# Optimization experiments

Measured on AMD Instinct MI355X. Metric: run time of the kernel, lower is better.

The kernel has to match this reference:

```python
import jax, jax.numpy as jnp
import numpy as np

B, L, D = 4, 2048, 256
DI, DS, DCONV, DTR, K = 512, 16, 4, 16, 3  # d_inner, d_state, mamba conv, dt_rank, outer conv kernel
PAD = 1 * (K - 1)  # dilation*(kernel_size-1)
ALPHA = 0.5


def setup_inputs() -> dict:
    key = jax.random.key(0)
    ks = jax.random.split(key, 14)
    s = lambda k, shape, scale: jax.random.normal(k, shape, dtype=jnp.float32) * scale
    inp = {
        "x": s(ks[0], (B, L, D), 1.0),
        "ln_w": jnp.ones((D,), jnp.float32),
        "ln_b": jnp.zeros((D,), jnp.float32),
        "conv_w": s(ks[1], (D, D, K), 0.05),          # outer Conv1d weight (out,in,k)
        "conv_b": s(ks[2], (D,), 0.02),
        "in_proj_w": s(ks[3], (2 * DI, D), 0.05),      # Mamba in_proj (no bias)
        "conv1d_w": s(ks[4], (DI, 1, DCONV), 0.3),     # depthwise causal conv
        "conv1d_b": s(ks[5], (DI,), 0.02),
        "x_proj_w": s(ks[6], (DTR + 2 * DS, DI), 0.05),
        "dt_proj_w": s(ks[7], (DI, DTR), 0.1),
        "dt_proj_b": s(ks[8], (DI,), 0.1),
        "A_log": jnp.log(jnp.broadcast_to(jnp.arange(1, DS + 1, dtype=jnp.float32), (DI, DS))),
        "D_param": jnp.ones((DI,), jnp.float32),
        "out_proj_w": s(ks[9], (D, DI), 0.05),
    }
    return inp


def _layernorm(h, w, b):
    mu = jnp.mean(h, axis=-1, keepdims=True)
    var = jnp.mean(jnp.square(h - mu), axis=-1, keepdims=True)
    return (h - mu) * jax.lax.rsqrt(var + 1e-5) * w + b


def _causal_conv(h_ncl, w, pad, groups):
    # h_ncl: (B, C, L); left-pad only -> output length L (matches pad-then-slice in torch)
    return jax.lax.conv_general_dilated(
        h_ncl, w, window_strides=(1,), padding=[(pad, 0)],
        dimension_numbers=("NCH", "OIH", "NCH"), feature_group_count=groups)


def _mamba(h, in_proj_w, conv1d_w, conv1d_b, x_proj_w, dt_proj_w, dt_proj_b, A_log, D_param, out_proj_w):
    xz = jnp.einsum("bld,ed->ble", h, in_proj_w)          # (B,L,2*DI)
    xin, z = jnp.split(xz, 2, axis=-1)
    xc = _causal_conv(xin.transpose(0, 2, 1), conv1d_w, DCONV - 1, DI)
    xc = jax.nn.silu(xc + conv1d_b[None, :, None]).transpose(0, 2, 1)   # (B,L,DI)
    x_dbl = jnp.einsum("bld,ed->ble", xc, x_proj_w)
    dt, Bm, Cm = jnp.split(x_dbl, [DTR, DTR + DS], axis=-1)
    delta = jax.nn.softplus(jnp.einsum("blr,dr->bld", dt, dt_proj_w) + dt_proj_b)  # (B,L,DI)
    A = -jnp.exp(A_log)                                     # (DI,DS)
    dA = jnp.exp(delta[..., None] * A)                      # (B,L,DI,DS)
    dBx = delta[..., None] * Bm[:, :, None, :] * xc[..., None]

    def step(hst, t):
        dA_t, dBx_t, C_t = t
        hst = dA_t * hst + dBx_t                            # (B,DI,DS)
        y = jnp.einsum("bds,bs->bd", hst, C_t)
        return hst, y

    h0 = jnp.zeros((h.shape[0], DI, DS), h.dtype)
    _, ys = jax.lax.scan(step, h0, (dA.transpose(1, 0, 2, 3), dBx.transpose(1, 0, 2, 3), Cm.transpose(1, 0, 2)))
    y = ys.transpose(1, 0, 2) + xc * D_param                # (B,L,DI)
    y = y * jax.nn.silu(z)
    return jnp.einsum("ble,de->bld", y, out_proj_w)


def reference(x, ln_w, ln_b, conv_w, conv_b, in_proj_w, conv1d_w, conv1d_b,
              x_proj_w, dt_proj_w, dt_proj_b, A_log, D_param, out_proj_w):
    h = _layernorm(x, ln_w, ln_b)
    # conv branch: pad left, conv, GELU (exact erf, as torch nn.GELU)
    hc = _causal_conv(h.transpose(0, 2, 1), conv_w, PAD, 1) + conv_b[None, :, None]
    h_conv = jax.nn.gelu(hc, approximate=False).transpose(0, 2, 1)
    h_mamba = _mamba(h, in_proj_w, conv1d_w, conv1d_b, x_proj_w, dt_proj_w,
                     dt_proj_b, A_log, D_param, out_proj_w)
    h_out = ALPHA * h_mamba + (1.0 - ALPHA) * h_conv
    return x + h_out
```

## Files before the change

kernel.cpp:

```cpp
#include <hip/hip_runtime.h>
#include <math.h>

#define BBATCH 4
#define LSEQ   2048
#define DMODEL 256
#define DINNER 512
#define DSTATE 16
#define DTRANK 16
#define MROWS  (BBATCH * LSEQ)
#define NCHUNK 64
#define LCHUNK (LSEQ / NCHUNK)

typedef unsigned short u16;
typedef __attribute__((ext_vector_type(8))) short bf16x8;
typedef __attribute__((ext_vector_type(4))) float f32x4;

#define OFF_HBF    ((size_t)0)
#define OFF_HCONV  ((size_t)1048576)
#define OFF_XIN    ((size_t)3145728)
#define OFF_XPART  ((size_t)5242880)
#define OFF_Z      ((size_t)7340032)
#define OFF_XC     ((size_t)11534336)
#define OFF_DELTA  ((size_t)15728640)
#define OFF_XDBL   ((size_t)19922944)
#define OFF_YBF    ((size_t)20316160)
#define OFF_AAGG   ((size_t)22413312)
#define OFF_BAGG   ((size_t)24510464)
#define OFF_HINIT  OFF_AAGG
#define OFF_WTINBF ((size_t)26607616)
#define OFF_WTCVBF ((size_t)26738688)
#define OFF_WTOUTBF ((size_t)26836992)
#define OFF_WTX    ((size_t)26902528)
#define OFF_WTDT   ((size_t)26927104)

__device__ __forceinline__ float silu_f(float v) {
  return v / (1.0f + __expf(-v));
}
__device__ __forceinline__ u16 f2bf(float f) {
  unsigned u = __float_as_uint(f);
  return (u16)((u + 0x7FFFu + ((u >> 16) & 1u)) >> 16);
}
__device__ __forceinline__ float bf2f(u16 v) {
  return __uint_as_float(((unsigned)v) << 16);
}

__global__ __launch_bounds__(256) void k_repack(
    const float* __restrict__ inw, const float* __restrict__ convw,
    const float* __restrict__ xw, const float* __restrict__ dtw,
    const float* __restrict__ ow, float* __restrict__ ws) {
  int idx = blockIdx.x * 256 + threadIdx.x;
  u16* win  = (u16*)(ws + OFF_WTINBF);
  u16* wcv  = (u16*)(ws + OFF_WTCVBF);
  u16* wout = (u16*)(ws + OFF_WTOUTBF);
  float* wx  = ws + OFF_WTX;
  float* wdt = ws + OFF_WTDT;
  if (idx < 262144) {
    win[idx] = f2bf(inw[idx]);
    return;
  }
  int i2 = idx - 262144;
  if (i2 < 196608) {
    int o = i2 / 768, r = i2 - o * 768;
    int kk = r >> 8, i = r & 255;
    wcv[i2] = f2bf(convw[(o * 256 + i) * 3 + kk]);
    return;
  }
  int i3 = i2 - 196608;
  if (i3 < 131072) {
    wout[i3] = f2bf(ow[i3]);
    return;
  }
  int i4 = i3 - 131072;
  if (i4 < 24576) {
    int k = i4 / 48, n = i4 - k * 48;
    wx[i4] = xw[n * 512 + k];
    return;
  }
  int i5 = i4 - 24576;
  if (i5 < 8192) {
    int r = i5 >> 9, n = i5 & 511;
    wdt[i5] = dtw[n * 16 + r];
  }
}

__global__ __launch_bounds__(256) void k_layernorm(
    const float* __restrict__ x, const float* __restrict__ w,
    const float* __restrict__ b, u16* __restrict__ hb) {
  int wave = threadIdx.x >> 6;
  int lane = threadIdx.x & 63;
  int row  = blockIdx.x * 4 + wave;
  const float4* xr = reinterpret_cast<const float4*>(x + (size_t)row * 256);
  float4 v = xr[lane];
  float s  = v.x + v.y + v.z + v.w;
  float sq = v.x*v.x + v.y*v.y + v.z*v.z + v.w*v.w;
  #pragma unroll
  for (int o = 32; o >= 1; o >>= 1) { s += __shfl_xor(s, o); sq += __shfl_xor(sq, o); }
  float mu  = s * (1.0f / 256.0f);
  float var = sq * (1.0f / 256.0f) - mu * mu;
  float rs  = rsqrtf(var + 1e-5f);
  float4 wv = reinterpret_cast<const float4*>(w)[lane];
  float4 bv = reinterpret_cast<const float4*>(b)[lane];
  ushort4 o4;
  o4.x = f2bf((v.x - mu) * rs * wv.x + bv.x);
  o4.y = f2bf((v.y - mu) * rs * wv.y + bv.y);
  o4.z = f2bf((v.z - mu) * rs * wv.z + bv.z);
  o4.w = f2bf((v.w - mu) * rs * wv.w + bv.w);
  reinterpret_cast<ushort4*>(hb + (size_t)row * 256)[lane] = o4;
}


__global__ __launch_bounds__(256) void k_bgemm_inproj(
    const u16* __restrict__ Abf, const u16* __restrict__ Bbf,
    u16* __restrict__ xin, u16* __restrict__ z) {
  __shared__ __align__(16) u16 As[64 * 72];
  __shared__ __align__(16) u16 Bs[128 * 72];
  int tid = threadIdx.x;
  int m0 = blockIdx.x * 64, n0 = blockIdx.y * 128;
  int lane = tid & 63, wid = tid >> 6;
  int wc = wid * 32;
  int l15 = lane & 15, lk = (lane >> 4) * 8;
  int r0 = tid >> 3, kc = (tid & 7) * 8;
  f32x4 acc[4][2] = {};
  for (int k0 = 0; k0 < 256; k0 += 64) {
    *(bf16x8*)&As[r0 * 72 + kc] =
        *(const bf16x8*)&Abf[(size_t)(m0 + r0) * 256 + k0 + kc];
    *(bf16x8*)&As[(r0 + 32) * 72 + kc] =
        *(const bf16x8*)&Abf[(size_t)(m0 + r0 + 32) * 256 + k0 + kc];
    #pragma unroll
    for (int rr = 0; rr < 4; ++rr)
      *(bf16x8*)&Bs[(r0 + rr * 32) * 72 + kc] =
          *(const bf16x8*)&Bbf[(size_t)(n0 + r0 + rr * 32) * 256 + k0 + kc];
    __syncthreads();
    #pragma unroll
    for (int kk = 0; kk < 64; kk += 32) {
      bf16x8 b0 = *(const bf16x8*)&Bs[(wc + l15) * 72 + kk + lk];
      bf16x8 b1 = *(const bf16x8*)&Bs[(wc + 16 + l15) * 72 + kk + lk];
      #pragma unroll
      for (int q = 0; q < 4; ++q) {
        bf16x8 a = *(const bf16x8*)&As[(q * 16 + l15) * 72 + kk + lk];
        acc[q][0] = __builtin_amdgcn_mfma_f32_16x16x32_bf16(a, b0, acc[q][0], 0, 0, 0);
        acc[q][1] = __builtin_amdgcn_mfma_f32_16x16x32_bf16(a, b1, acc[q][1], 0, 0, 0);
      }
    }
    __syncthreads();
  }
  u16* dst = (blockIdx.y < 4) ? xin : z;
  int nb = n0 & 511;
  int rsub = (lane >> 4) * 4;
  #pragma unroll
  for (int q = 0; q < 4; ++q)
    #pragma unroll
    for (int ni = 0; ni < 2; ++ni) {
      int gc = nb + wc + ni * 16 + l15;
      #pragma unroll
      for (int r = 0; r < 4; ++r)
        dst[(size_t)(m0 + q * 16 + rsub + r) * 512 + gc] = f2bf(acc[q][ni][r]);
    }
}

__global__ __launch_bounds__(256) void k_bgemm_conv(
    const u16* __restrict__ hbf, const u16* __restrict__ Bbf,
    const float* __restrict__ cb, float* __restrict__ hconv) {
  __shared__ __align__(16) u16 As[64 * 72];
  __shared__ __align__(16) u16 Bs[64 * 72];
  int tid = threadIdx.x;
  int m0 = blockIdx.x * 64, n0 = blockIdx.y * 64;
  int bidx = m0 >> 11, t0 = m0 & 2047;
  int lane = tid & 63, wid = tid >> 6;
  int wr = (wid >> 1) * 32, wc = (wid & 1) * 32;
  int l15 = lane & 15, lk = (lane >> 4) * 8;
  int r0 = tid >> 3, kc = (tid & 7) * 8;
  f32x4 acc[2][2] = {};
  for (int k0 = 0; k0 < 768; k0 += 64) {
    int kkc = k0 >> 8;
    int i0  = (k0 & 255) + kc;
    int t1  = t0 + r0 - 2 + kkc;
    bf16x8 av0 = {0, 0, 0, 0, 0, 0, 0, 0};
    if (t1 >= 0)
      av0 = *(const bf16x8*)&hbf[(size_t)((bidx << 11) + t1) * 256 + i0];
    bf16x8 av1 =
        *(const bf16x8*)&hbf[(size_t)((bidx << 11) + t1 + 32) * 256 + i0];
    *(bf16x8*)&As[r0 * 72 + kc] = av0;
    *(bf16x8*)&As[(r0 + 32) * 72 + kc] = av1;
    *(bf16x8*)&Bs[r0 * 72 + kc] =
        *(const bf16x8*)&Bbf[(size_t)(n0 + r0) * 768 + k0 + kc];
    *(bf16x8*)&Bs[(r0 + 32) * 72 + kc] =
        *(const bf16x8*)&Bbf[(size_t)(n0 + r0 + 32) * 768 + k0 + kc];
    __syncthreads();
    #pragma unroll
    for (int kk = 0; kk < 64; kk += 32) {
      bf16x8 a0 = *(const bf16x8*)&As[(wr + l15) * 72 + kk + lk];
      bf16x8 a1 = *(const bf16x8*)&As[(wr + 16 + l15) * 72 + kk + lk];
      bf16x8 b0 = *(const bf16x8*)&Bs[(wc + l15) * 72 + kk + lk];
      bf16x8 b1 = *(const bf16x8*)&Bs[(wc + 16 + l15) * 72 + kk + lk];
      acc[0][0] = __builtin_amdgcn_mfma_f32_16x16x32_bf16(a0, b0, acc[0][0], 0, 0, 0);
      acc[0][1] = __builtin_amdgcn_mfma_f32_16x16x32_bf16(a0, b1, acc[0][1], 0, 0, 0);
      acc[1][0] = __builtin_amdgcn_mfma_f32_16x16x32_bf16(a1, b0, acc[1][0], 0, 0, 0);
      acc[1][1] = __builtin_amdgcn_mfma_f32_16x16x32_bf16(a1, b1, acc[1][1], 0, 0, 0);
    }
    __syncthreads();
  }
  int rowb = m0 + wr + (lane >> 4) * 4;
  #pragma unroll
  for (int mi = 0; mi < 2; ++mi)
    #pragma unroll
    for (int ni = 0; ni < 2; ++ni) {
      int gc = n0 + wc + ni * 16 + l15;
      float bias = cb[gc];
      #pragma unroll
      for (int r = 0; r < 4; ++r) {
        float v = acc[mi][ni][r] + bias;
        float g = 0.5f * v * (1.0f + erff(v * 0.70710678118654752440f));
        hconv[(size_t)(rowb + mi * 16 + r) * 256 + gc] = g;
      }
    }
}

__global__ __launch_bounds__(256) void k_bgemm_outproj(
    const u16* __restrict__ Abf, const u16* __restrict__ Bbf,
    const float* __restrict__ x, const float* __restrict__ hconv,
    float* __restrict__ out) {
  __shared__ __align__(16) u16 As[64 * 72];
  __shared__ __align__(16) u16 Bs[64 * 72];
  int tid = threadIdx.x;
  int m0 = blockIdx.x * 64, n0 = blockIdx.y * 64;
  int lane = tid & 63, wid = tid >> 6;
  int wr = (wid >> 1) * 32, wc = (wid & 1) * 32;
  int l15 = lane & 15, lk = (lane >> 4) * 8;
  int r0 = tid >> 3, kc = (tid & 7) * 8;
  f32x4 acc[2][2] = {};
  for (int k0 = 0; k0 < 512; k0 += 64) {
    *(bf16x8*)&As[r0 * 72 + kc] =
        *(const bf16x8*)&Abf[(size_t)(m0 + r0) * 512 + k0 + kc];
    *(bf16x8*)&As[(r0 + 32) * 72 + kc] =
        *(const bf16x8*)&Abf[(size_t)(m0 + r0 + 32) * 512 + k0 + kc];
    *(bf16x8*)&Bs[r0 * 72 + kc] =
        *(const bf16x8*)&Bbf[(size_t)(n0 + r0) * 512 + k0 + kc];
    *(bf16x8*)&Bs[(r0 + 32) * 72 + kc] =
        *(const bf16x8*)&Bbf[(size_t)(n0 + r0 + 32) * 512 + k0 + kc];
    __syncthreads();
    #pragma unroll
    for (int kk = 0; kk < 64; kk += 32) {
      bf16x8 a0 = *(const bf16x8*)&As[(wr + l15) * 72 + kk + lk];
      bf16x8 a1 = *(const bf16x8*)&As[(wr + 16 + l15) * 72 + kk + lk];
      bf16x8 b0 = *(const bf16x8*)&Bs[(wc + l15) * 72 + kk + lk];
      bf16x8 b1 = *(const bf16x8*)&Bs[(wc + 16 + l15) * 72 + kk + lk];
      acc[0][0] = __builtin_amdgcn_mfma_f32_16x16x32_bf16(a0, b0, acc[0][0], 0, 0, 0);
      acc[0][1] = __builtin_amdgcn_mfma_f32_16x16x32_bf16(a0, b1, acc[0][1], 0, 0, 0);
      acc[1][0] = __builtin_amdgcn_mfma_f32_16x16x32_bf16(a1, b0, acc[1][0], 0, 0, 0);
      acc[1][1] = __builtin_amdgcn_mfma_f32_16x16x32_bf16(a1, b1, acc[1][1], 0, 0, 0);
    }
    __syncthreads();
  }
  int rowb = m0 + wr + (lane >> 4) * 4;
  #pragma unroll
  for (int mi = 0; mi < 2; ++mi)
    #pragma unroll
    for (int ni = 0; ni < 2; ++ni) {
      int gc = n0 + wc + ni * 16 + l15;
      #pragma unroll
      for (int r = 0; r < 4; ++r) {
        size_t off = (size_t)(rowb + mi * 16 + r) * 256 + gc;
        out[off] = x[off] + 0.5f * acc[mi][ni][r] + 0.5f * hconv[off];
      }
    }
}

__global__ __launch_bounds__(256) void k_xproj_part(
    const float* __restrict__ A, const float* __restrict__ Bt,
    float* __restrict__ Cpart) {
  __shared__ float As[16][68];
  __shared__ float Bs[16][68];
  int tid = threadIdx.x;
  int m0 = blockIdx.x * 64;
  int kc = blockIdx.y;
  int ar = tid >> 2, ac = (tid & 3) * 4;
  int br = tid >> 4, bc = (tid & 15) * 4;
  int tx = tid & 15, ty = tid >> 4;
  float acc[4][4] = {};
  for (int k0 = kc * 128; k0 < kc * 128 + 128; k0 += 16) {
    float4 av = *reinterpret_cast<const float4*>(A + (size_t)(m0 + ar) * 512 + k0 + ac);
    As[ac + 0][ar] = av.x; As[ac + 1][ar] = av.y;
    As[ac + 2][ar] = av.z; As[ac + 3][ar] = av.w;
    float4 bv = make_float4(0.f, 0.f, 0.f, 0.f);
    if (bc < 48)
      bv = *reinterpret_cast<const float4*>(Bt + (size_t)(k0 + br) * 48 + bc);
    *reinterpret_cast<float4*>(&Bs[br][bc]) = bv;
    __syncthreads();
    #pragma unroll
    for (int kt = 0; kt < 16; ++kt) {
      float4 a = *reinterpret_cast<const float4*>(&As[kt][ty * 4]);
      float4 b = *reinterpret_cast<const float4*>(&Bs[kt][tx * 4]);
      acc[0][0]+=a.x*b.x; acc[0][1]+=a.x*b.y; acc[0][2]+=a.x*b.z; acc[0][3]+=a.x*b.w;
      acc[1][0]+=a.y*b.x; acc[1][1]+=a.y*b.y; acc[1][2]+=a.y*b.z; acc[1][3]+=a.y*b.w;
      acc[2][0]+=a.z*b.x; acc[2][1]+=a.z*b.y; acc[2][2]+=a.z*b.z; acc[2][3]+=a.z*b.w;
      acc[3][0]+=a.w*b.x; acc[3][1]+=a.w*b.y; acc[3][2]+=a.w*b.z; acc[3][3]+=a.w*b.w;
    }
    __syncthreads();
  }
  float* C = Cpart + (size_t)kc * (MROWS * 48);
  if (tx < 12) {
    #pragma unroll
    for (int i = 0; i < 4; ++i) {
      float4 cv = make_float4(acc[i][0], acc[i][1], acc[i][2], acc[i][3]);
      *reinterpret_cast<float4*>(C + (size_t)(m0 + ty * 4 + i) * 48 + tx * 4) = cv;
    }
  }
}

__global__ __launch_bounds__(256) void k_xproj_sum(
    const float* __restrict__ Cpart, float* __restrict__ C) {
  int idx = blockIdx.x * 256 + threadIdx.x;
  const size_t S = (size_t)MROWS * 48;
  C[idx] = ((Cpart[idx] + Cpart[S + idx]) + Cpart[2 * S + idx]) + Cpart[3 * S + idx];
}

__global__ __launch_bounds__(256) void k_dtproj(
    const float* __restrict__ xdbl, const float* __restrict__ Wdt,
    const float* __restrict__ db, float* __restrict__ delta) {
  __shared__ float dts[4][17];
  int tid = threadIdx.x;
  int m0 = blockIdx.x * 4;
  if (tid < 64) {
    int rr = tid >> 4, cc = tid & 15;
    dts[rr][cc] = xdbl[(size_t)(m0 + rr) * 48 + cc];
  }
  __syncthreads();
  float wv0[16], wv1[16];
  #pragma unroll
  for (int r = 0; r < 16; ++r) {
    wv0[r] = Wdt[r * 512 + tid];
    wv1[r] = Wdt[r * 512 + tid + 256];
  }
  float b0 = db[tid], b1 = db[tid + 256];
  #pragma unroll
  for (int m = 0; m < 4; ++m) {
    float a0 = b0, a1 = b1;
    #pragma unroll
    for (int r = 0; r < 16; ++r) {
      float d = dts[m][r];
      a0 += d * wv0[r];
      a1 += d * wv1[r];
    }
    delta[(size_t)(m0 + m) * 512 + tid]       = (a0 > 20.0f) ? a0 : log1pf(__expf(a0));
    delta[(size_t)(m0 + m) * 512 + tid + 256] = (a1 > 20.0f) ? a1 : log1pf(__expf(a1));
  }
}

__global__ __launch_bounds__(256) void k_dwconv(
    const u16* __restrict__ xin, const float* __restrict__ cw,
    const float* __restrict__ cb, float* __restrict__ xc) {
  int idx = blockIdx.x * 256 + threadIdx.x;
  int di = idx & 511;
  int m  = idx >> 9;
  int t  = m & 2047;
  float w0 = cw[di * 4 + 0], w1 = cw[di * 4 + 1];
  float w2 = cw[di * 4 + 2], w3 = cw[di * 4 + 3];
  const u16* base = xin + (size_t)m * 512 + di;
  float acc = cb[di] + w3 * bf2f(base[0]);
  if (t >= 1) acc += w2 * bf2f(base[-512]);
  if (t >= 2) acc += w1 * bf2f(base[-1024]);
  if (t >= 3) acc += w0 * bf2f(base[-1536]);
  xc[(size_t)m * 512 + di] = silu_f(acc);
}

__global__ __launch_bounds__(256) void k_scan1(
    const float* __restrict__ delta, const float* __restrict__ xdbl,
    const float* __restrict__ xc, const float* __restrict__ Alog,
    float* __restrict__ Aagg, float* __restrict__ Bagg) {
  int di = ((blockIdx.x & 1) << 8) | threadIdx.x;
  int c  = (blockIdx.x >> 1) & 63;
  int b  = blockIdx.x >> 7;
  float nA[16];
  #pragma unroll
  for (int q = 0; q < 4; ++q) {
    float4 v = *reinterpret_cast<const float4*>(Alog + (size_t)di * 16 + q * 4);
    nA[q*4+0] = -__expf(v.x); nA[q*4+1] = -__expf(v.y);
    nA[q*4+2] = -__expf(v.z); nA[q*4+3] = -__expf(v.w);
  }
  float ap[16], bacc[16];
  #pragma unroll
  for (int s = 0; s < 16; ++s) { ap[s] = 1.0f; bacc[s] = 0.0f; }
  int row0 = b * 2048 + c * LCHUNK;
  const float* dp = delta + (size_t)row0 * 512 + di;
  const float* xp = xc    + (size_t)row0 * 512 + di;
  const float* Bp = xdbl  + (size_t)row0 * 48 + 16;
  #pragma unroll 2
  for (int t = 0; t < LCHUNK; ++t) {
    float dv = dp[t * 512];
    float u  = dv * xp[t * 512];
    #pragma unroll
    for (int s = 0; s < 16; ++s) {
      float e = __expf(dv * nA[s]);
      ap[s]   *= e;
      bacc[s]  = e * bacc[s] + u * Bp[t * 48 + s];
    }
  }
  size_t base = ((size_t)((b * 64 + c) * 16)) * 512 + di;
  #pragma unroll
  for (int s = 0; s < 16; ++s) {
    Aagg[base + (size_t)s * 512] = ap[s];
    Bagg[base + (size_t)s * 512] = bacc[s];
  }
}

__global__ __launch_bounds__(256) void k_scan2(
    const float* __restrict__ Aagg, const float* __restrict__ Bagg,
    float* __restrict__ Hinit) {
  int g  = blockIdx.x * 256 + threadIdx.x;
  int di = g & 511, s = (g >> 9) & 15, b = g >> 13;
  float h = 0.0f;
  for (int c = 0; c < NCHUNK; ++c) {
    size_t idx = ((size_t)((b * 64 + c) * 16 + s)) * 512 + di;
    float a = Aagg[idx], bb = Bagg[idx];
    Hinit[idx] = h;
    h = a * h + bb;
  }
}

__global__ __launch_bounds__(256) void k_scan3(
    const float* __restrict__ delta, const float* __restrict__ xdbl,
    const float* __restrict__ xc, const u16* __restrict__ z,
    const float* __restrict__ Alog, const float* __restrict__ Dp,
    const float* __restrict__ Hinit, u16* __restrict__ y) {
  int di = ((blockIdx.x & 1) << 8) | threadIdx.x;
  int c  = (blockIdx.x >> 1) & 63;
  int b  = blockIdx.x >> 7;
  float nA[16];
  #pragma unroll
  for (int q = 0; q < 4; ++q) {
    float4 v = *reinterpret_cast<const float4*>(Alog + (size_t)di * 16 + q * 4);
    nA[q*4+0] = -__expf(v.x); nA[q*4+1] = -__expf(v.y);
    nA[q*4+2] = -__expf(v.z); nA[q*4+3] = -__expf(v.w);
  }
  float h[16];
  size_t hb = ((size_t)((b * 64 + c) * 16)) * 512 + di;
  #pragma unroll
  for (int s = 0; s < 16; ++s) h[s] = Hinit[hb + (size_t)s * 512];
  float Dv = Dp[di];
  int row0 = b * 2048 + c * LCHUNK;
  const float* dp = delta + (size_t)row0 * 512 + di;
  const float* xp = xc    + (size_t)row0 * 512 + di;
  const u16*   zp = z     + (size_t)row0 * 512 + di;
  const float* Bp = xdbl  + (size_t)row0 * 48 + 16;
  const float* Cp = xdbl  + (size_t)row0 * 48 + 32;
  u16* yp         = y     + (size_t)row0 * 512 + di;
  #pragma unroll 2
  for (int t = 0; t < LCHUNK; ++t) {
    float dv  = dp[t * 512];
    float xcv = xp[t * 512];
    float u   = dv * xcv;
    float yv  = 0.0f;
    #pragma unroll
    for (int s = 0; s < 16; ++s) {
      float e = __expf(dv * nA[s]);
      h[s] = e * h[s] + u * Bp[t * 48 + s];
      yv  += h[s] * Cp[t * 48 + s];
    }
    yv += xcv * Dv;
    float zv = bf2f(zp[t * 512]);
    yp[t * 512] = f2bf(yv * silu_f(zv));
  }
}

extern "C" void kernel_launch(void* const* d_in, const int* in_sizes, int n_in,
                              void* d_out, int out_size, void* d_ws, size_t ws_size,
                              hipStream_t stream) {
  const float* x     = (const float*)d_in[0];
  const float* lnw   = (const float*)d_in[1];
  const float* lnb   = (const float*)d_in[2];
  const float* convw = (const float*)d_in[3];
  const float* convb = (const float*)d_in[4];
  const float* inw   = (const float*)d_in[5];
  const float* c1w   = (const float*)d_in[6];
  const float* c1b   = (const float*)d_in[7];
  const float* xw    = (const float*)d_in[8];
  const float* dtw   = (const float*)d_in[9];
  const float* dtb   = (const float*)d_in[10];
  const float* alog  = (const float*)d_in[11];
  const float* Dp    = (const float*)d_in[12];
  const float* ow    = (const float*)d_in[13];
  float* ws  = (float*)d_ws;
  float* out = (float*)d_out;

  u16* hbf     = (u16*)(ws + OFF_HBF);
  float* hconv = ws + OFF_HCONV;
  u16* xinbf   = (u16*)(ws + OFF_XIN);
  float* xpart = ws + OFF_XPART;
  u16* zbf     = (u16*)(ws + OFF_Z);
  float* xc    = ws + OFF_XC;
  float* delta = ws + OFF_DELTA;
  float* xdbl  = ws + OFF_XDBL;
  u16* ybf     = (u16*)(ws + OFF_YBF);
  float* Aagg  = ws + OFF_AAGG;
  float* Bagg  = ws + OFF_BAGG;
  float* Hinit = ws + OFF_HINIT;
  u16* winbf   = (u16*)(ws + OFF_WTINBF);
  u16* wcvbf   = (u16*)(ws + OFF_WTCVBF);
  u16* woutbf  = (u16*)(ws + OFF_WTOUTBF);
  float* Wtx   = ws + OFF_WTX;
  float* Wtdt  = ws + OFF_WTDT;

  k_repack<<<2432, 256, 0, stream>>>(inw, convw, xw, dtw, ow, ws);
  k_layernorm<<<2048, 256, 0, stream>>>(x, lnw, lnb, hbf);
  k_bgemm_conv<<<dim3(128, 4), 256, 0, stream>>>(hbf, wcvbf, convb, hconv);
  k_bgemm_inproj<<<dim3(128, 8), 256, 0, stream>>>(hbf, winbf, xinbf, zbf);
  k_dwconv<<<16384, 256, 0, stream>>>(xinbf, c1w, c1b, xc);
  k_xproj_part<<<dim3(128, 4), 256, 0, stream>>>(xc, Wtx, xpart);
  k_xproj_sum<<<1536, 256, 0, stream>>>(xpart, xdbl);
  k_dtproj<<<2048, 256, 0, stream>>>(xdbl, Wtdt, dtb, delta);
  k_scan1<<<512, 256, 0, stream>>>(delta, xdbl, xc, alog, Aagg, Bagg);
  k_scan2<<<128, 256, 0, stream>>>(Aagg, Bagg, Hinit);
  k_scan3<<<512, 256, 0, stream>>>(delta, xdbl, xc, zbf, alog, Dp, Hinit, ybf);
  k_bgemm_outproj<<<dim3(128, 4), 256, 0, stream>>>(ybf, woutbf, x, hconv, out);
}
```

Before: 237.9 us.

## Merge layernorm with weight repack, fuse conv/inproj GEMMs, fold xproj reduction into dtproj

Three launch-level fusions. Layernorm and weight repacking now run as one grid split by block index. The conv-branch GEMM and the in_proj GEMM run as one grid, also split by block index. The split-K partial sum for x_proj is folded into the dt_proj kernel, which also writes xdbl. This removes three kernel launches, the gaps between them, and one intermediate pass over the x_proj partials. The risk is that the merged GEMM kernel now reserves the larger shared-memory footprint for conv blocks as well, which could lower occupancy.

Result: faster. 218.9 us (-8.0%).

```diff
diff --git a/kernel.cpp b/kernel.cpp
--- a/kernel.cpp
+++ b/kernel.cpp
@@ -44,11 +44,36 @@
   return __uint_as_float(((unsigned)v) << 16);
 }
 
-__global__ __launch_bounds__(256) void k_repack(
+__global__ __launch_bounds__(256) void k_ln_repack(
+    const float* __restrict__ x, const float* __restrict__ lnw,
+    const float* __restrict__ lnb, u16* __restrict__ hb,
     const float* __restrict__ inw, const float* __restrict__ convw,
     const float* __restrict__ xw, const float* __restrict__ dtw,
     const float* __restrict__ ow, float* __restrict__ ws) {
-  int idx = blockIdx.x * 256 + threadIdx.x;
+  if (blockIdx.x < 2048) {
+    int wave = threadIdx.x >> 6;
+    int lane = threadIdx.x & 63;
+    int row  = blockIdx.x * 4 + wave;
+    const float4* xr = reinterpret_cast<const float4*>(x + (size_t)row * 256);
+    float4 v = xr[lane];
+    float s  = v.x + v.y + v.z + v.w;
+    float sq = v.x*v.x + v.y*v.y + v.z*v.z + v.w*v.w;
+    #pragma unroll
+    for (int o = 32; o >= 1; o >>= 1) { s += __shfl_xor(s, o); sq += __shfl_xor(sq, o); }
+    float mu  = s * (1.0f / 256.0f);
+    float var = sq * (1.0f / 256.0f) - mu * mu;
+    float rs  = rsqrtf(var + 1e-5f);
+    float4 wv = reinterpret_cast<const float4*>(lnw)[lane];
+    float4 bv = reinterpret_cast<const float4*>(lnb)[lane];
+    ushort4 o4;
+    o4.x = f2bf((v.x - mu) * rs * wv.x + bv.x);
+    o4.y = f2bf((v.y - mu) * rs * wv.y + bv.y);
+    o4.z = f2bf((v.z - mu) * rs * wv.z + bv.z);
+    o4.w = f2bf((v.w - mu) * rs * wv.w + bv.w);
+    reinterpret_cast<ushort4*>(hb + (size_t)row * 256)[lane] = o4;
+    return;
+  }
+  int idx = (blockIdx.x - 2048) * 256 + threadIdx.x;
   u16* win  = (u16*)(ws + OFF_WTINBF);
   u16* wcv  = (u16*)(ws + OFF_WTCVBF);
   u16* wout = (u16*)(ws + OFF_WTOUTBF);
@@ -83,53 +108,82 @@
   }
 }
 
-__global__ __launch_bounds__(256) void k_layernorm(
-    const float* __restrict__ x, const float* __restrict__ w,
-    const float* __restrict__ b, u16* __restrict__ hb) {
-  int wave = threadIdx.x >> 6;
-  int lane = threadIdx.x & 63;
-  int row  = blockIdx.x * 4 + wave;
-  const float4* xr = reinterpret_cast<const float4*>(x + (size_t)row * 256);
-  float4 v = xr[lane];
-  float s  = v.x + v.y + v.z + v.w;
-  float sq = v.x*v.x + v.y*v.y + v.z*v.z + v.w*v.w;
-  #pragma unroll
-  for (int o = 32; o >= 1; o >>= 1) { s += __shfl_xor(s, o); sq += __shfl_xor(sq, o); }
-  float mu  = s * (1.0f / 256.0f);
-  float var = sq * (1.0f / 256.0f) - mu * mu;
-  float rs  = rsqrtf(var + 1e-5f);
-  float4 wv = reinterpret_cast<const float4*>(w)[lane];
-  float4 bv = reinterpret_cast<const float4*>(b)[lane];
-  ushort4 o4;
-  o4.x = f2bf((v.x - mu) * rs * wv.x + bv.x);
-  o4.y = f2bf((v.y - mu) * rs * wv.y + bv.y);
-  o4.z = f2bf((v.z - mu) * rs * wv.z + bv.z);
-  o4.w = f2bf((v.w - mu) * rs * wv.w + bv.w);
-  reinterpret_cast<ushort4*>(hb + (size_t)row * 256)[lane] = o4;
-}
-
-
-__global__ __launch_bounds__(256) void k_bgemm_inproj(
-    const u16* __restrict__ Abf, const u16* __restrict__ Bbf,
-    u16* __restrict__ xin, u16* __restrict__ z) {
+
+__global__ __launch_bounds__(256) void k_bgemm_both(
+    const u16* __restrict__ hbf, const u16* __restrict__ Bcv,
+    const float* __restrict__ cb, float* __restrict__ hconv,
+    const u16* __restrict__ Bin, u16* __restrict__ xin, u16* __restrict__ z) {
   __shared__ __align__(16) u16 As[64 * 72];
   __shared__ __align__(16) u16 Bs[128 * 72];
+  int blk = blockIdx.x;
   int tid = threadIdx.x;
-  int m0 = blockIdx.x * 64, n0 = blockIdx.y * 128;
   int lane = tid & 63, wid = tid >> 6;
-  int wc = wid * 32;
   int l15 = lane & 15, lk = (lane >> 4) * 8;
   int r0 = tid >> 3, kc = (tid & 7) * 8;
+  if (blk < 512) {
+    int m0 = (blk & 127) * 64, n0 = (blk >> 7) * 64;
+    int bidx = m0 >> 11, t0 = m0 & 2047;
+    int wr = (wid >> 1) * 32, wc = (wid & 1) * 32;
+    f32x4 acc[2][2] = {};
+    for (int k0 = 0; k0 < 768; k0 += 64) {
+      int kkc = k0 >> 8;
+      int i0  = (k0 & 255) + kc;
+      int t1  = t0 + r0 - 2 + kkc;
+      bf16x8 av0 = {0, 0, 0, 0, 0, 0, 0, 0};
+      if (t1 >= 0)
+        av0 = *(const bf16x8*)&hbf[(size_t)((bidx << 11) + t1) * 256 + i0];
+      bf16x8 av1 =
+          *(const bf16x8*)&hbf[(size_t)((bidx << 11) + t1 + 32) * 256 + i0];
+      *(bf16x8*)&As[r0 * 72 + kc] = av0;
+      *(bf16x8*)&As[(r0 + 32) * 72 + kc] = av1;
+      *(bf16x8*)&Bs[r0 * 72 + kc] =
+          *(const bf16x8*)&Bcv[(size_t)(n0 + r0) * 768 + k0 + kc];
+      *(bf16x8*)&Bs[(r0 + 32) * 72 + kc] =
+          *(const bf16x8*)&Bcv[(size_t)(n0 + r0 + 32) * 768 + k0 + kc];
+      __syncthreads();
+      #pragma unroll
+      for (int kk = 0; kk < 64; kk += 32) {
+        bf16x8 a0 = *(const bf16x8*)&As[(wr + l15) * 72 + kk + lk];
+        bf16x8 a1 = *(const bf16x8*)&As[(wr + 16 + l15) * 72 + kk + lk];
+        bf16x8 b0 = *(const bf16x8*)&Bs[(wc + l15) * 72 + kk + lk];
+        bf16x8 b1 = *(const bf16x8*)&Bs[(wc + 16 + l15) * 72 + kk + lk];
+        acc[0][0] = __builtin_amdgcn_mfma_f32_16x16x32_bf16(a0, b0, acc[0][0], 0, 0, 0);
+        acc[0][1] = __builtin_amdgcn_mfma_f32_16x16x32_bf16(a0, b1, acc[0][1], 0, 0, 0);
+        acc[1][0] = __builtin_amdgcn_mfma_f32_16x16x32_bf16(a1, b0, acc[1][0], 0, 0, 0);
+        acc[1][1] = __builtin_amdgcn_mfma_f32_16x16x32_bf16(a1, b1, acc[1][1], 0, 0, 0);
+      }
+      __syncthreads();
+    }
+    int rowb = m0 + wr + (lane >> 4) * 4;
+    #pragma unroll
+    for (int mi = 0; mi < 2; ++mi)
+      #pragma unroll
+      for (int ni = 0; ni < 2; ++ni) {
+        int gc = n0 + wc + ni * 16 + l15;
+        float bias = cb[gc];
+        #pragma unroll
+        for (int r = 0; r < 4; ++r) {
+          float v = acc[mi][ni][r] + bias;
+          float g = 0.5f * v * (1.0f + erff(v * 0.70710678118654752440f));
+          hconv[(size_t)(rowb + mi * 16 + r) * 256 + gc] = g;
+        }
+      }
+    return;
+  }
+  int bid = blk - 512;
+  int m0 = (bid & 127) * 64, ny = bid >> 7;
+  int n0 = ny * 128;
+  int wc = wid * 32;
   f32x4 acc[4][2] = {};
   for (int k0 = 0; k0 < 256; k0 += 64) {
     *(bf16x8*)&As[r0 * 72 + kc] =
-        *(const bf16x8*)&Abf[(size_t)(m0 + r0) * 256 + k0 + kc];
+        *(const bf16x8*)&hbf[(size_t)(m0 + r0) * 256 + k0 + kc];
     *(bf16x8*)&As[(r0 + 32) * 72 + kc] =
-        *(const bf16x8*)&Abf[(size_t)(m0 + r0 + 32) * 256 + k0 + kc];
+        *(const bf16x8*)&hbf[(size_t)(m0 + r0 + 32) * 256 + k0 + kc];
     #pragma unroll
     for (int rr = 0; rr < 4; ++rr)
       *(bf16x8*)&Bs[(r0 + rr * 32) * 72 + kc] =
-          *(const bf16x8*)&Bbf[(size_t)(n0 + r0 + rr * 32) * 256 + k0 + kc];
+          *(const bf16x8*)&Bin[(size_t)(n0 + r0 + rr * 32) * 256 + k0 + kc];
     __syncthreads();
     #pragma unroll
     for (int kk = 0; kk < 64; kk += 32) {
@@ -144,7 +198,7 @@
     }
     __syncthreads();
   }
-  u16* dst = (blockIdx.y < 4) ? xin : z;
+  u16* dst = (ny < 4) ? xin : z;
   int nb = n0 & 511;
   int rsub = (lane >> 4) * 4;
   #pragma unroll
@@ -155,64 +209,6 @@
       #pragma unroll
       for (int r = 0; r < 4; ++r)
         dst[(size_t)(m0 + q * 16 + rsub + r) * 512 + gc] = f2bf(acc[q][ni][r]);
-    }
-}
-
-__global__ __launch_bounds__(256) void k_bgemm_conv(
-    const u16* __restrict__ hbf, const u16* __restrict__ Bbf,
-    const float* __restrict__ cb, float* __restrict__ hconv) {
-  __shared__ __align__(16) u16 As[64 * 72];
-  __shared__ __align__(16) u16 Bs[64 * 72];
-  int tid = threadIdx.x;
-  int m0 = blockIdx.x * 64, n0 = blockIdx.y * 64;
-  int bidx = m0 >> 11, t0 = m0 & 2047;
-  int lane = tid & 63, wid = tid >> 6;
-  int wr = (wid >> 1) * 32, wc = (wid & 1) * 32;
-  int l15 = lane & 15, lk = (lane >> 4) * 8;
-  int r0 = tid >> 3, kc = (tid & 7) * 8;
-  f32x4 acc[2][2] = {};
-  for (int k0 = 0; k0 < 768; k0 += 64) {
-    int kkc = k0 >> 8;
-    int i0  = (k0 & 255) + kc;
-    int t1  = t0 + r0 - 2 + kkc;
-    bf16x8 av0 = {0, 0, 0, 0, 0, 0, 0, 0};
-    if (t1 >= 0)
-      av0 = *(const bf16x8*)&hbf[(size_t)((bidx << 11) + t1) * 256 + i0];
-    bf16x8 av1 =
-        *(const bf16x8*)&hbf[(size_t)((bidx << 11) + t1 + 32) * 256 + i0];
-    *(bf16x8*)&As[r0 * 72 + kc] = av0;
-    *(bf16x8*)&As[(r0 + 32) * 72 + kc] = av1;
-    *(bf16x8*)&Bs[r0 * 72 + kc] =
-        *(const bf16x8*)&Bbf[(size_t)(n0 + r0) * 768 + k0 + kc];
-    *(bf16x8*)&Bs[(r0 + 32) * 72 + kc] =
-        *(const bf16x8*)&Bbf[(size_t)(n0 + r0 + 32) * 768 + k0 + kc];
-    __syncthreads();
-    #pragma unroll
-    for (int kk = 0; kk < 64; kk += 32) {
-      bf16x8 a0 = *(const bf16x8*)&As[(wr + l15) * 72 + kk + lk];
-      bf16x8 a1 = *(const bf16x8*)&As[(wr + 16 + l15) * 72 + kk + lk];
-      bf16x8 b0 = *(const bf16x8*)&Bs[(wc + l15) * 72 + kk + lk];
-      bf16x8 b1 = *(const bf16x8*)&Bs[(wc + 16 + l15) * 72 + kk + lk];
-      acc[0][0] = __builtin_amdgcn_mfma_f32_16x16x32_bf16(a0, b0, acc[0][0], 0, 0, 0);
-      acc[0][1] = __builtin_amdgcn_mfma_f32_16x16x32_bf16(a0, b1, acc[0][1], 0, 0, 0);
-      acc[1][0] = __builtin_amdgcn_mfma_f32_16x16x32_bf16(a1, b0, acc[1][0], 0, 0, 0);
-      acc[1][1] = __builtin_amdgcn_mfma_f32_16x16x32_bf16(a1, b1, acc[1][1], 0, 0, 0);
-    }
-    __syncthreads();
-  }
-  int rowb = m0 + wr + (lane >> 4) * 4;
-  #pragma unroll
-  for (int mi = 0; mi < 2; ++mi)
-    #pragma unroll
-    for (int ni = 0; ni < 2; ++ni) {
-      int gc = n0 + wc + ni * 16 + l15;
-      float bias = cb[gc];
-      #pragma unroll
-      for (int r = 0; r < 4; ++r) {
-        float v = acc[mi][ni][r] + bias;
-        float g = 0.5f * v * (1.0f + erff(v * 0.70710678118654752440f));
-        hconv[(size_t)(rowb + mi * 16 + r) * 256 + gc] = g;
-      }
     }
 }
 
@@ -308,22 +304,20 @@
   }
 }
 
-__global__ __launch_bounds__(256) void k_xproj_sum(
-    const float* __restrict__ Cpart, float* __restrict__ C) {
-  int idx = blockIdx.x * 256 + threadIdx.x;
-  const size_t S = (size_t)MROWS * 48;
-  C[idx] = ((Cpart[idx] + Cpart[S + idx]) + Cpart[2 * S + idx]) + Cpart[3 * S + idx];
-}
-
 __global__ __launch_bounds__(256) void k_dtproj(
-    const float* __restrict__ xdbl, const float* __restrict__ Wdt,
-    const float* __restrict__ db, float* __restrict__ delta) {
+    const float* __restrict__ Cpart, const float* __restrict__ Wdt,
+    const float* __restrict__ db, float* __restrict__ xdbl,
+    float* __restrict__ delta) {
   __shared__ float dts[4][17];
   int tid = threadIdx.x;
   int m0 = blockIdx.x * 4;
-  if (tid < 64) {
-    int rr = tid >> 4, cc = tid & 15;
-    dts[rr][cc] = xdbl[(size_t)(m0 + rr) * 48 + cc];
+  const size_t S = (size_t)MROWS * 48;
+  if (tid < 192) {
+    int rr = tid / 48, cc = tid - rr * 48;
+    size_t off = (size_t)(m0 + rr) * 48 + cc;
+    float v = ((Cpart[off] + Cpart[S + off]) + Cpart[2 * S + off]) + Cpart[3 * S + off];
+    xdbl[off] = v;
+    if (cc < 16) dts[rr][cc] = v;
   }
   __syncthreads();
   float wv0[16], wv1[16];
@@ -501,14 +495,13 @@
   float* Wtx   = ws + OFF_WTX;
   float* Wtdt  = ws + OFF_WTDT;
 
-  k_repack<<<2432, 256, 0, stream>>>(inw, convw, xw, dtw, ow, ws);
-  k_layernorm<<<2048, 256, 0, stream>>>(x, lnw, lnb, hbf);
-  k_bgemm_conv<<<dim3(128, 4), 256, 0, stream>>>(hbf, wcvbf, convb, hconv);
-  k_bgemm_inproj<<<dim3(128, 8), 256, 0, stream>>>(hbf, winbf, xinbf, zbf);
+  k_ln_repack<<<4480, 256, 0, stream>>>(x, lnw, lnb, hbf,
+                                        inw, convw, xw, dtw, ow, ws);
+  k_bgemm_both<<<1536, 256, 0, stream>>>(hbf, wcvbf, convb, hconv,
+                                         winbf, xinbf, zbf);
   k_dwconv<<<16384, 256, 0, stream>>>(xinbf, c1w, c1b, xc);
   k_xproj_part<<<dim3(128, 4), 256, 0, stream>>>(xc, Wtx, xpart);
-  k_xproj_sum<<<1536, 256, 0, stream>>>(xpart, xdbl);
-  k_dtproj<<<2048, 256, 0, stream>>>(xdbl, Wtdt, dtb, delta);
+  k_dtproj<<<2048, 256, 0, stream>>>(xpart, Wtdt, dtb, xdbl, delta);
   k_scan1<<<512, 256, 0, stream>>>(delta, xdbl, xc, alog, Aagg, Bagg);
   k_scan2<<<128, 256, 0, stream>>>(Aagg, Bagg, Hinit);
   k_scan3<<<512, 256, 0, stream>>>(delta, xdbl, xc, zbf, alog, Dp, Hinit, ybf);
```
